# Kernel optimization log

Measured on AMD Instinct MI355X. Metric: run time of the kernel, lower is better.

Reference implementation:

```python
import jax, jax.numpy as jnp
import numpy as np

VOCAB, EMB, HID, OUT = 50257, 256, 512, 2

def setup_inputs() -> dict:
    key = jax.random.key(0)
    ks = jax.random.split(key, 8)
    s_e = 1.0  # nn.Embedding default N(0,1)
    emb = jax.random.normal(ks[0], (VOCAB, EMB), dtype=jnp.float32) * s_e
    emb = emb.at[0].set(0.0)  # padding_idx=0
    def lin(k1, k2, fan_in, fan_out):
        bound = 1.0 / np.sqrt(fan_in)
        w = jax.random.uniform(k1, (fan_out, fan_in), minval=-bound, maxval=bound, dtype=jnp.float32)
        b = jax.random.uniform(k2, (fan_out,), minval=-bound, maxval=bound, dtype=jnp.float32)
        return w, b
    Ww, Wb = lin(ks[1], ks[2], EMB, HID)
    Uw, Ub = lin(ks[3], ks[4], HID, HID)
    Vw, Vb = lin(ks[5], ks[6], HID, OUT)
    x = jax.random.randint(ks[7], (128, 512), 0, VOCAB, dtype=jnp.int64)
    return {"x": x, "emb": emb, "Ww": Ww, "Wb": Wb, "Uw": Uw, "Ub": Ub, "Vw": Vw, "Vb": Vb}

def reference(x, emb, Ww, Wb, Uw, Ub, Vw, Vb):
    # x: [B, T] int tokens -> embed: [B, T, E]
    xe = emb[x]
    # Precompute input projections for all timesteps in one big GEMM: [B, T, H]
    wx = jnp.einsum('bte,he->bth', xe, Ww) + Wb
    B = x.shape[0]
    h0 = jnp.zeros((B, Uw.shape[0]), dtype=xe.dtype)
    def step(h, wx_t):
        h_new = jnp.tanh(wx_t + h @ Uw.T + Ub)
        return h_new, None
    hT, _ = jax.lax.scan(step, h0, jnp.swapaxes(wx, 0, 1))  # scan over time [T, B, H]
    logits = hT @ Vw.T + Vb  # [B, OUT]
    return logits
```

## Files before the change

kernel.cpp:

```cpp
#include <hip/hip_runtime.h>
#include <hip/hip_bf16.h>
#include <math.h>


#define VOCAB   50257
#define T_STEPS 512
#define HID     512
#define EMB     256

typedef __bf16 bf16x8 __attribute__((ext_vector_type(8)));
typedef float  f32x4  __attribute__((ext_vector_type(4)));
typedef float  f32x2  __attribute__((ext_vector_type(2)));
typedef int    i32x4  __attribute__((ext_vector_type(4)));

__device__ inline float ldf(const void* p, long i, bool f32) {
    if (f32) return ((const float*)p)[i];
    unsigned bits = ((unsigned)((const unsigned short*)p)[i]) << 16;
    return __uint_as_float(bits);
}
__device__ inline void stf(void* p, long i, float v, bool f32) {
    if (f32) { ((float*)p)[i] = v; return; }
    unsigned b = __float_as_uint(v);
    unsigned r = (b + 0x7fffu + ((b >> 16) & 1u)) >> 16;
    ((unsigned short*)p)[i] = (unsigned short)r;
}
__device__ inline unsigned short f2bf(float v) {
    unsigned b = __float_as_uint(v);
    return (unsigned short)((b + 0x7fffu + ((b >> 16) & 1u)) >> 16);
}
__device__ inline float bf2f(unsigned short u) {
    return __uint_as_float(((unsigned)u) << 16);
}
__device__ inline int get_tok(const int* x, int idx, bool x64) {
    unsigned u = (unsigned)(x64 ? x[2 * idx] : x[idx]);
    return (u < (unsigned)VOCAB) ? (int)u : 0;
}
__device__ inline int detect_flags(const int* x, const void* emb) {
    int allz = 1;
    const unsigned short* e16 = (const unsigned short*)emb;
    for (int i = 256; i < 320; ++i) allz &= (e16[i] == 0);
    int x64 = 1;
    for (int j = 1; j < 16; j += 2) x64 &= (x[j] == 0);
    return allz | (x64 << 1);
}
__device__ inline float tanh_f(float x) {
    float ax = fabsf(x);
    float e  = __expf(-2.0f * ax);
    float t  = (1.0f - e) * __builtin_amdgcn_rcpf(1.0f + e);
    return copysignf(t, x);
}
__device__ inline unsigned tq(float v) {
    float x = fminf(3.5f, fmaxf(-3.5f, v));
    float s = x * x;
    float num = x * fmaf(s, fmaf(s, 127.0f, 13335.0f), 120015.0f);
    float den = fmaf(s, fmaf(s, 15.0f, 420.0f), 945.0f);
    float f = fmaf(num, __builtin_amdgcn_rcpf(den), 12582912.0f);
    return __float_as_uint(f) & 0xffu;
}
__device__ inline unsigned tq2(float a, float b) {
    f32x2 x;
    x.x = fminf(3.5f, fmaxf(-3.5f, a));
    x.y = fminf(3.5f, fmaxf(-3.5f, b));
    f32x2 s   = x * x;
    f32x2 num = x * (s * (s * 127.0f + 13335.0f) + 120015.0f);
    f32x2 den = s * (s * 15.0f + 420.0f) + 945.0f;
    float f0 = fmaf(num.x, __builtin_amdgcn_rcpf(den.x), 12582912.0f);
    float f1 = fmaf(num.y, __builtin_amdgcn_rcpf(den.y), 12582912.0f);
    return __builtin_amdgcn_perm(__float_as_uint(f1), __float_as_uint(f0),
                                 0x0c0c0400u);
}

#define XEPAD 264
__global__ __launch_bounds__(1024) void wx_gemm(
    const int* __restrict__ x, const void* __restrict__ embv,
    const void* __restrict__ Wwv, const void* __restrict__ Wbv,
    const void* __restrict__ Ubv, unsigned char* __restrict__ ws)
{
    __shared__ __align__(16) __hip_bfloat16 xe_s[64][XEPAD];
    __shared__ int flags_s;
    const int t = blockIdx.x, tid = threadIdx.x;
    if (tid == 0) flags_s = detect_flags(x, embv);
    __syncthreads();
    const bool f32w = (flags_s & 1) != 0;
    const bool x64  = (flags_s & 2) != 0;

    const int w = tid >> 6, lane = tid & 63, ln = lane & 15, q = lane >> 4;

    bf16x8 bf[2][8];
    float  bias[2];
#pragma unroll
    for (int tn = 0; tn < 2; ++tn) {
        long n = w * 32 + tn * 16 + ln;
        bias[tn] = ldf(Wbv, n, f32w) + ldf(Ubv, n, f32w);
#pragma unroll
        for (int kt = 0; kt < 8; ++kt) {
            bf16x8 v;
            if (f32w) {
                const float4* p = (const float4*)((const float*)Wwv
                                    + n * EMB + kt * 32 + q * 8);
                float4 a = p[0], b = p[1];
                v[0] = (__bf16)a.x; v[1] = (__bf16)a.y;
                v[2] = (__bf16)a.z; v[3] = (__bf16)a.w;
                v[4] = (__bf16)b.x; v[5] = (__bf16)b.y;
                v[6] = (__bf16)b.z; v[7] = (__bf16)b.w;
            } else {
                v = *(const bf16x8*)((const unsigned short*)Wwv
                                    + n * EMB + kt * 32 + q * 8);
            }
            bf[tn][kt] = v;
        }
    }

    for (int half = 0; half < 2; ++half) {
        {
            int row = tid >> 4, sub = tid & 15;
            int tok = get_tok(x, (half * 64 + row) * T_STEPS + t, x64);
#pragma unroll
            for (int i = 0; i < 4; ++i) {
                int col = sub * 4 + i * 64;
                __hip_bfloat16* d = &xe_s[row][col];
                if (f32w) {
                    const float4 vv = *(const float4*)((const float*)embv
                                        + (long)tok * EMB + col);
                    d[0] = __float2bfloat16(vv.x); d[1] = __float2bfloat16(vv.y);
                    d[2] = __float2bfloat16(vv.z); d[3] = __float2bfloat16(vv.w);
                } else {
                    *(uint2*)d = *(const uint2*)((const unsigned short*)embv
                                        + (long)tok * EMB + col);
                }
            }
        }
        __syncthreads();

#pragma unroll
        for (int bt = 0; bt < 4; ++bt) {
            f32x4 acc[2];
#pragma unroll
            for (int tn = 0; tn < 2; ++tn)
#pragma unroll
                for (int r = 0; r < 4; ++r) acc[tn][r] = bias[tn];
#pragma unroll
            for (int kt = 0; kt < 8; ++kt) {
                bf16x8 a = *(const bf16x8*)&xe_s[bt * 16 + ln][kt * 32 + q * 8];
#pragma unroll
                for (int tn = 0; tn < 2; ++tn)
                    acc[tn] = __builtin_amdgcn_mfma_f32_16x16x32_bf16(
                        a, bf[tn][kt], acc[tn], 0, 0, 0);
            }
            {
                int g = half * 4 + bt;
                unsigned short o8[8];
#pragma unroll
                for (int tn = 0; tn < 2; ++tn)
#pragma unroll
                    for (int r = 0; r < 4; ++r)
                        o8[tn * 4 + r] = f2bf(acc[tn][r]);
                long ofs = (((long)t * 8 + g) * 1024 + tid) * 16;
                *(uint4*)(ws + ofs) = *(const uint4*)o8;
            }
        }
        __syncthreads();
    }
}

#define HQP 528
__global__ __launch_bounds__(1024) void scan_i8(
    const void* __restrict__ Uwv, const void* __restrict__ Vwv,
    const void* __restrict__ Vbv, const int* __restrict__ x,
    const void* __restrict__ embv, const unsigned char* __restrict__ wsc,
    void* __restrict__ outv)
{
    __shared__ __align__(16) signed char hq[2][16][HQP];
    __shared__ float red[1024];
    __shared__ int flags_s;

    const int tid = threadIdx.x, g = blockIdx.x, b0 = g * 16;
    if (tid == 0) flags_s = detect_flags(x, embv);
    __syncthreads();
    const bool f32w = (flags_s & 1) != 0;

    const int w = tid >> 6, lane = tid & 63, ln = lane & 15, q = lane >> 4;

    {
        float mx = 0.0f;
        if (f32w) {
            const float4* U4 = (const float4*)Uwv;
            for (int i = tid; i < 65536; i += 1024) {
                float4 v = U4[i];
                mx = fmaxf(mx, fmaxf(fmaxf(fabsf(v.x), fabsf(v.y)),
                                     fmaxf(fabsf(v.z), fabsf(v.w))));
            }
        } else {
            for (long i = tid; i < 262144; i += 1024)
                mx = fmaxf(mx, fabsf(ldf(Uwv, i, false)));
        }
        red[tid] = mx;
        __syncthreads();
        for (int s = 512; s > 0; s >>= 1) {
            if (tid < s) red[tid] = fmaxf(red[tid], red[tid + s]);
            __syncthreads();
        }
    }
    const float su = red[0];
    const float qs = 127.0f / su;
    const float sc = su / 16129.0f;

    i32x4 uq[2][8];
#pragma unroll
    for (int tn = 0; tn < 2; ++tn) {
        long n = w * 32 + tn * 16 + ln;
#pragma unroll
        for (int kt = 0; kt < 8; ++kt) {
            i32x4 frag;
#pragma unroll
            for (int wd = 0; wd < 4; ++wd) {
                unsigned pk = 0;
#pragma unroll
                for (int jb = 0; jb < 4; ++jb) {
                    int kp = kt * 64 + q * 16 + wd * 4 + jb;
                    int kl = (kp & ~31) | ((kp & 1) << 4) | ((kp >> 1) & 15);
                    float v = ldf(Uwv, n * HID + kl, f32w) * qs;
                    int   qv = (int)__builtin_rintf(v);
                    qv = qv > 127 ? 127 : (qv < -127 ? -127 : qv);
                    pk |= ((unsigned)(unsigned char)(signed char)qv) << (8 * jb);
                }
                frag[wd] = (int)pk;
            }
            uq[tn][kt] = frag;
        }
    }

    for (int i = tid; i < 16 * HQP; i += 1024) ((signed char*)hq[0])[i] = 0;
    __syncthreads();

    const unsigned char* wxp = wsc + ((long)g * 1024 + tid) * 16;
    const long wx_step = 8L * 1024 * 16;

    uint4 wv = *(const uint4*)wxp;
    const unsigned char* wp = wxp + wx_step;

    for (int t = 0; t < T_STEPS; ++t) {
        uint4 wvn = *(const uint4*)((t + 1 < T_STEPS) ? wp : wxp);
        wp += wx_step;

        i32x4 acc0 = {0, 0, 0, 0}, acc1 = {0, 0, 0, 0};
        const signed char (*hr)[HQP] = hq[t & 1];
#pragma unroll
        for (int ktb = 0; ktb < 2; ++ktb) {
            i32x4 afr[4];
#pragma unroll
            for (int k = 0; k < 4; ++k)
                afr[k] = *(const i32x4*)&hr[ln][(ktb * 4 + k) * 64 + q * 16];
#pragma unroll
            for (int k = 0; k < 4; ++k) {
                acc0 = __builtin_amdgcn_mfma_i32_16x16x64_i8(
                    afr[k], uq[0][ktb * 4 + k], acc0, 0, 0, 0);
                acc1 = __builtin_amdgcn_mfma_i32_16x16x64_i8(
                    afr[k], uq[1][ktb * 4 + k], acc1, 0, 0, 0);
            }
        }

        float wx0[4], wx1[4];
        wx0[0] = __uint_as_float(wv.x << 16); wx0[1] = __uint_as_float(wv.x & 0xffff0000u);
        wx0[2] = __uint_as_float(wv.y << 16); wx0[3] = __uint_as_float(wv.y & 0xffff0000u);
        wx1[0] = __uint_as_float(wv.z << 16); wx1[1] = __uint_as_float(wv.z & 0xffff0000u);
        wx1[2] = __uint_as_float(wv.w << 16); wx1[3] = __uint_as_float(wv.w & 0xffff0000u);

        signed char (*hw)[HQP] = hq[(t + 1) & 1];
#pragma unroll
        for (int r = 0; r < 4; ++r) {
            unsigned c01 = tq2(fmaf((float)acc0[r], sc, wx0[r]),
                               fmaf((float)acc1[r], sc, wx1[r]));
            *(unsigned short*)&hw[q * 4 + r][w * 32 + ln * 2] =
                (unsigned short)c01;
        }
        asm volatile("s_waitcnt lgkmcnt(0)" ::: "memory");
        __builtin_amdgcn_s_barrier();
        wv = wvn;
    }

    if (tid < 512) {
        int b = tid >> 5, o = (tid >> 4) & 1, kp = tid & 15;
        float s = 0.0f;
#pragma unroll 4
        for (int j = 0; j < 32; ++j) {
            int kph = kp * 32 + j;
            int kl = (kph & ~31) | ((kph & 1) << 4) | ((kph >> 1) & 15);
            s += (float)hq[0][b][kph] * (1.0f / 127.0f)
               * ldf(Vwv, (long)o * HID + kl, f32w);
        }
        s += __shfl_xor(s, 1);
        s += __shfl_xor(s, 2);
        s += __shfl_xor(s, 4);
        s += __shfl_xor(s, 8);
        if (kp == 0)
            stf(outv, (long)(b0 + b) * 2 + o, s + ldf(Vbv, o, f32w), f32w);
    }
}

#define XPAD 264
#define HPAD 528
#define BPG  4
#define R7_WS_H   4096
#define R7_WS_NEED (4096 + 2 * 8 * 16 * 256 * 4)

__device__ inline void load_xe(const void* emb, long base, bool f32,
                               bf16x8* a, bf16x8* b) {
    if (f32) {
        const float* p = (const float*)emb + base;
        bf16x8 va, vb;
#pragma unroll
        for (int j = 0; j < 8; ++j) va[j] = (__bf16)p[j];
#pragma unroll
        for (int j = 0; j < 8; ++j) vb[j] = (__bf16)p[8 + j];
        *a = va; *b = vb;
    } else {
        const bf16x8* p = (const bf16x8*)((const unsigned short*)emb + base);
        *a = p[0]; *b = p[1];
    }
}

__global__ __launch_bounds__(256, 1) void scan_mfma_fb(
    const int* __restrict__ x, const void* __restrict__ embv,
    const void* __restrict__ Wwv, const void* __restrict__ Wbv,
    const void* __restrict__ Uwv, const void* __restrict__ Ubv,
    const void* __restrict__ Vwv, const void* __restrict__ Vbv,
    unsigned char* __restrict__ ws, void* __restrict__ outv)
{
    __shared__ __align__(16) __hip_bfloat16 xe_s[16][XPAD];
    __shared__ __align__(16) __hip_bfloat16 hbuf[2][16][HPAD];
    __shared__ int flags_s;

    const int tid = threadIdx.x;
    const int g   = blockIdx.x >> 2;
    const int cg  = blockIdx.x & 3;
    const int b0  = g * 16;

    if (tid == 0) flags_s = detect_flags(x, embv);
    __syncthreads();
    const bool f32w = (flags_s & 1) != 0;
    const bool x64  = (flags_s & 2) != 0;

    const int w = tid >> 6, lane = tid & 63, ln = lane & 15, q = lane >> 4;
    const int n0 = cg * 128 + w * 32 + ln;

    for (int i = tid; i < 2 * 16 * HPAD; i += 256)
        ((__hip_bfloat16*)hbuf)[i] = __float2bfloat16(0.0f);

    bf16x8 ufr[2][16], wfr[2][8];
#pragma unroll
    for (int half = 0; half < 2; ++half) {
        const long n = n0 + half * 16;
#pragma unroll
        for (int kt = 0; kt < 16; ++kt) {
            bf16x8 v;
#pragma unroll
            for (int j = 0; j < 8; ++j)
                v[j] = (__bf16)ldf(Uwv, n * HID + kt * 32 + q * 8 + j, f32w);
            ufr[half][kt] = v;
        }
#pragma unroll
        for (int kt = 0; kt < 8; ++kt) {
            bf16x8 v;
#pragma unroll
            for (int j = 0; j < 8; ++j)
                v[j] = (__bf16)ldf(Wwv, n * EMB + kt * 32 + q * 8 + j, f32w);
            wfr[half][kt] = v;
        }
    }
    const float bias0 = ldf(Wbv, n0, f32w)      + ldf(Ubv, n0, f32w);
    const float bias1 = ldf(Wbv, n0 + 16, f32w) + ldf(Ubv, n0 + 16, f32w);

    const int xr = tid >> 4, xc = (tid & 15) * 16;
    {
        int tok = get_tok(x, (b0 + xr) * T_STEPS + 0, x64);
        bf16x8 xa, xb;
        load_xe(embv, (long)tok * EMB + xc, f32w, &xa, &xb);
        *(bf16x8*)&xe_s[xr][xc]     = xa;
        *(bf16x8*)&xe_s[xr][xc + 8] = xb;
    }
    __syncthreads();

    unsigned*           hg32 = (unsigned*)(ws + R7_WS_H);
    unsigned long long* hg64 = (unsigned long long*)(ws + R7_WS_H);
    int*                cnt  = (int*)(void*)ws + g * 32;

    for (int t = 0; t < T_STEPS; ++t) {
        bf16x8 nxa, nxb;
        const bool have_next = (t + 1 < T_STEPS);
        if (have_next) {
            int tok = get_tok(x, (b0 + xr) * T_STEPS + (t + 1), x64);
            load_xe(embv, (long)tok * EMB + xc, f32w, &nxa, &nxb);
        }

        f32x4 acc0, acc1;
#pragma unroll
        for (int r = 0; r < 4; ++r) { acc0[r] = bias0; acc1[r] = bias1; }
#pragma unroll
        for (int kt = 0; kt < 8; ++kt) {
            bf16x8 a = *(const bf16x8*)&xe_s[ln][kt * 32 + q * 8];
            acc0 = __builtin_amdgcn_mfma_f32_16x16x32_bf16(a, wfr[0][kt], acc0, 0, 0, 0);
            acc1 = __builtin_amdgcn_mfma_f32_16x16x32_bf16(a, wfr[1][kt], acc1, 0, 0, 0);
        }
        const __hip_bfloat16 (*hr)[HPAD] = hbuf[t & 1];
#pragma unroll
        for (int kt = 0; kt < 16; ++kt) {
            bf16x8 a = *(const bf16x8*)&hr[ln][kt * 32 + q * 8];
            acc0 = __builtin_amdgcn_mfma_f32_16x16x32_bf16(a, ufr[0][kt], acc0, 0, 0, 0);
            acc1 = __builtin_amdgcn_mfma_f32_16x16x32_bf16(a, ufr[1][kt], acc1, 0, 0, 0);
        }

        const int nb = (t + 1) & 1;
        {
            unsigned* dst = hg32 + (size_t)(nb * 8 + g) * 4096 + cg * 64 + w * 16 + ln;
#pragma unroll
            for (int r = 0; r < 4; ++r) {
                unsigned word = (unsigned)f2bf(tanh_f(acc0[r]))
                              | ((unsigned)f2bf(tanh_f(acc1[r])) << 16);
                __hip_atomic_store(dst + (size_t)(q * 4 + r) * 256, word,
                                   __ATOMIC_RELAXED, __HIP_MEMORY_SCOPE_AGENT);
            }
        }
        asm volatile("s_waitcnt vmcnt(0)" ::: "memory");
        __syncthreads();

        if (have_next) {
            *(bf16x8*)&xe_s[xr][xc]     = nxa;
            *(bf16x8*)&xe_s[xr][xc + 8] = nxb;
        }

        if (tid == 0) {
            __hip_atomic_fetch_add(cnt, 1, __ATOMIC_RELAXED,
                                   __HIP_MEMORY_SCOPE_AGENT);
            const int target = BPG * (t + 1);
            while (__hip_atomic_load(cnt, __ATOMIC_RELAXED,
                                     __HIP_MEMORY_SCOPE_AGENT) < target)
                __builtin_amdgcn_s_sleep(1);
        }
        __syncthreads();

        {
            const unsigned long long* src = hg64 + (size_t)(nb * 8 + g) * 2048;
#pragma unroll
            for (int m = tid; m < 2048; m += 256) {
                unsigned long long v = __hip_atomic_load(
                    src + m, __ATOMIC_RELAXED, __HIP_MEMORY_SCOPE_AGENT);
                int row = m >> 7, p = m & 127;
                int j0  = 2 * p;
                int cgp = j0 >> 6, wv = (j0 >> 4) & 3, l0 = j0 & 15;
                int colA = cgp * 128 + wv * 32 + l0;
                unsigned w0 = (unsigned)v, w1 = (unsigned)(v >> 32);
                unsigned lo = (w0 & 0xffffu) | (w1 << 16);
                unsigned hi = (w0 >> 16) | (w1 & 0xffff0000u);
                *(unsigned*)&hbuf[nb][row][colA]      = lo;
                *(unsigned*)&hbuf[nb][row][colA + 16] = hi;
            }
        }
        __syncthreads();
    }

    if (cg == 0) {
        int b = tid >> 4, rem = tid & 15, o = rem >> 3, kp = rem & 7;
        float s = 0.0f;
#pragma unroll 4
        for (int j = 0; j < 64; ++j) {
            int k = kp * 64 + j;
            s += __bfloat162float(hbuf[0][b][k]) * ldf(Vwv, (long)o * HID + k, f32w);
        }
        s += __shfl_xor(s, 1);
        s += __shfl_xor(s, 2);
        s += __shfl_xor(s, 4);
        if (kp == 0)
            stf(outv, (long)(b0 + b) * 2 + o, s + ldf(Vbv, o, f32w), f32w);
    }
}

#define B_PER 2
__global__ __launch_bounds__(512) void fixup(
    const int* __restrict__ x, const void* __restrict__ emb,
    const void* __restrict__ Ww, const void* __restrict__ Wb,
    const void* __restrict__ Uw, const void* __restrict__ Ub,
    const void* __restrict__ Vw, const void* __restrict__ Vb,
    void* __restrict__ out, int force)
{
    __shared__ float h_s[2][B_PER][HID];
    __shared__ float xe_sf[B_PER][EMB];
    __shared__ int   flags_s, bad_s;

    const int tid = threadIdx.x;
    const int b0  = blockIdx.x * B_PER;

    if (tid == 0) {
        int fl = detect_flags(x, emb);
        flags_s = fl;
        int bad = force;
        if (!force) {
            bool f32o = (fl & 1) != 0;
            for (int i = 0; i < 2 * B_PER; ++i) {
                int oi = b0 * 2 + i;
                if (f32o) {
                    float v = ((const float*)out)[oi];
                    bad |= (v != v);
                } else {
                    unsigned short u = ((const unsigned short*)out)[oi];
                    bad |= (((u & 0x7F80u) == 0x7F80u) && ((u & 0x7Fu) != 0));
                }
            }
        }
        bad_s = bad;
    }
    __syncthreads();
    if (!bad_s) return;

    const bool f32w = (flags_s & 1) != 0;
    const bool x64  = (flags_s & 2) != 0;
    const int n = tid;
    const float bias = ldf(Wb, n, f32w) + ldf(Ub, n, f32w);

    for (int b = 0; b < B_PER; ++b) h_s[0][b][n] = 0.0f;

    for (int t = 0; t < T_STEPS; ++t) {
        {
            int b = tid >> 8, c = tid & 255;
            int tok = get_tok(x, (b0 + b) * T_STEPS + t, x64);
            xe_sf[b][c] = ldf(emb, (long)tok * EMB + c, f32w);
        }
        __syncthreads();

        float acc0 = bias, acc1 = bias;
        const long wrow = (long)n * EMB;
#pragma unroll 8
        for (int k = 0; k < EMB; ++k) {
            float wv = ldf(Ww, wrow + k, f32w);
            acc0 += xe_sf[0][k] * wv;
            acc1 += xe_sf[1][k] * wv;
        }
        const long urow = (long)n * HID;
        const float* hc0 = h_s[t & 1][0];
        const float* hc1 = h_s[t & 1][1];
#pragma unroll 8
        for (int k = 0; k < HID; ++k) {
            float uv = ldf(Uw, urow + k, f32w);
            acc0 += hc0[k] * uv;
            acc1 += hc1[k] * uv;
        }
        h_s[(t + 1) & 1][0][n] = tanhf(acc0);
        h_s[(t + 1) & 1][1][n] = tanhf(acc1);
        __syncthreads();
    }

    if (tid < 2 * B_PER) {
        int b = tid >> 1, o = tid & 1;
        float s = ldf(Vb, o, f32w);
        for (int k = 0; k < HID; ++k)
            s += h_s[0][b][k] * ldf(Vw, (long)o * HID + k, f32w);
        stf(out, (b0 + b) * 2 + o, s, f32w);
    }
}

extern "C" void kernel_launch(void* const* d_in, const int* in_sizes, int n_in,
                              void* d_out, int out_size, void* d_ws, size_t ws_size,
                              hipStream_t stream) {
    const int* x = (const int*)d_in[0];
    const size_t WX16 = (size_t)T_STEPS * 128 * 512 * 2;
    if (ws_size >= WX16) {
        wx_gemm<<<512, 1024, 0, stream>>>(
            x, d_in[1], d_in[2], d_in[3], d_in[5], (unsigned char*)d_ws);
        scan_i8<<<8, 1024, 0, stream>>>(
            d_in[4], d_in[6], d_in[7], x, d_in[1],
            (const unsigned char*)d_ws, d_out);
        fixup<<<64, 512, 0, stream>>>(
            x, d_in[1], d_in[2], d_in[3], d_in[4], d_in[5], d_in[6], d_in[7],
            d_out, 0);
    } else if (ws_size >= (size_t)R7_WS_NEED) {
        hipMemsetAsync(d_ws, 0, 4096, stream);
        scan_mfma_fb<<<32, 256, 0, stream>>>(
            x, d_in[1], d_in[2], d_in[3], d_in[4], d_in[5], d_in[6], d_in[7],
            (unsigned char*)d_ws, d_out);
        fixup<<<64, 512, 0, stream>>>(
            x, d_in[1], d_in[2], d_in[3], d_in[4], d_in[5], d_in[6], d_in[7],
            d_out, 0);
    } else {
        fixup<<<64, 512, 0, stream>>>(
            x, d_in[1], d_in[2], d_in[3], d_in[4], d_in[5], d_in[6], d_in[7],
            d_out, 1);
    }
}
```

Measured before the change: 857.3 us.

## Overlap tanh epilogue with second MFMA chain and load all embeddings in one pass

```diff
diff --git a/kernel.cpp b/kernel.cpp
--- a/kernel.cpp
+++ b/kernel.cpp
@@ -76,7 +76,7 @@
     const void* __restrict__ Wwv, const void* __restrict__ Wbv,
     const void* __restrict__ Ubv, unsigned char* __restrict__ ws)
 {
-    __shared__ __align__(16) __hip_bfloat16 xe_s[64][XEPAD];
+    __shared__ __align__(16) __hip_bfloat16 xe_s[128][XEPAD];
     __shared__ int flags_s;
     const int t = blockIdx.x, tid = threadIdx.x;
     if (tid == 0) flags_s = detect_flags(x, embv);
@@ -85,6 +85,30 @@
     const bool x64  = (flags_s & 2) != 0;
 
     const int w = tid >> 6, lane = tid & 63, ln = lane & 15, q = lane >> 4;
+
+    {
+        int row = tid >> 3, sub = tid & 7;
+        int tok = get_tok(x, row * T_STEPS + t, x64);
+        if (f32w) {
+            const float* src = (const float*)embv + (long)tok * EMB;
+#pragma unroll
+            for (int i = 0; i < 8; ++i) {
+                int col = sub * 4 + i * 32;
+                float4 vv = *(const float4*)(src + col);
+                __hip_bfloat16* d = &xe_s[row][col];
+                d[0] = __float2bfloat16(vv.x); d[1] = __float2bfloat16(vv.y);
+                d[2] = __float2bfloat16(vv.z); d[3] = __float2bfloat16(vv.w);
+            }
+        } else {
+            const unsigned short* src = (const unsigned short*)embv
+                                      + (long)tok * EMB;
+#pragma unroll
+            for (int i = 0; i < 4; ++i) {
+                int col = sub * 8 + i * 64;
+                *(uint4*)&xe_s[row][col] = *(const uint4*)(src + col);
+            }
+        }
+    }
 
     bf16x8 bf[2][8];
     float  bias[2];
@@ -110,56 +134,33 @@
             bf[tn][kt] = v;
         }
     }
-
-    for (int half = 0; half < 2; ++half) {
+    __syncthreads();
+
+#pragma unroll
+    for (int bt = 0; bt < 8; ++bt) {
+        f32x4 acc[2];
+#pragma unroll
+        for (int tn = 0; tn < 2; ++tn)
+#pragma unroll
+            for (int r = 0; r < 4; ++r) acc[tn][r] = bias[tn];
+#pragma unroll
+        for (int kt = 0; kt < 8; ++kt) {
+            bf16x8 a = *(const bf16x8*)&xe_s[bt * 16 + ln][kt * 32 + q * 8];
+#pragma unroll
+            for (int tn = 0; tn < 2; ++tn)
+                acc[tn] = __builtin_amdgcn_mfma_f32_16x16x32_bf16(
+                    a, bf[tn][kt], acc[tn], 0, 0, 0);
+        }
         {
-            int row = tid >> 4, sub = tid & 15;
-            int tok = get_tok(x, (half * 64 + row) * T_STEPS + t, x64);
-#pragma unroll
-            for (int i = 0; i < 4; ++i) {
-                int col = sub * 4 + i * 64;
-                __hip_bfloat16* d = &xe_s[row][col];
-                if (f32w) {
-                    const float4 vv = *(const float4*)((const float*)embv
-                                        + (long)tok * EMB + col);
-                    d[0] = __float2bfloat16(vv.x); d[1] = __float2bfloat16(vv.y);
-                    d[2] = __float2bfloat16(vv.z); d[3] = __float2bfloat16(vv.w);
-                } else {
-                    *(uint2*)d = *(const uint2*)((const unsigned short*)embv
-                                        + (long)tok * EMB + col);
-                }
-            }
-        }
-        __syncthreads();
-
-#pragma unroll
-        for (int bt = 0; bt < 4; ++bt) {
-            f32x4 acc[2];
+            unsigned short o8[8];
 #pragma unroll
             for (int tn = 0; tn < 2; ++tn)
 #pragma unroll
-                for (int r = 0; r < 4; ++r) acc[tn][r] = bias[tn];
-#pragma unroll
-            for (int kt = 0; kt < 8; ++kt) {
-                bf16x8 a = *(const bf16x8*)&xe_s[bt * 16 + ln][kt * 32 + q * 8];
-#pragma unroll
-                for (int tn = 0; tn < 2; ++tn)
-                    acc[tn] = __builtin_amdgcn_mfma_f32_16x16x32_bf16(
-                        a, bf[tn][kt], acc[tn], 0, 0, 0);
-            }
-            {
-                int g = half * 4 + bt;
-                unsigned short o8[8];
-#pragma unroll
-                for (int tn = 0; tn < 2; ++tn)
-#pragma unroll
-                    for (int r = 0; r < 4; ++r)
-                        o8[tn * 4 + r] = f2bf(acc[tn][r]);
-                long ofs = (((long)t * 8 + g) * 1024 + tid) * 16;
-                *(uint4*)(ws + ofs) = *(const uint4*)o8;
-            }
-        }
-        __syncthreads();
+                for (int r = 0; r < 4; ++r)
+                    o8[tn * 4 + r] = f2bf(acc[tn][r]);
+            long ofs = (((long)t * 8 + bt) * 1024 + tid) * 16;
+            *(uint4*)(ws + ofs) = *(const uint4*)o8;
+        }
     }
 }
 
@@ -239,26 +240,11 @@
     uint4 wv = *(const uint4*)wxp;
     const unsigned char* wp = wxp + wx_step;
 
+    const int wcol = w * 32 + ln * 2;
+
     for (int t = 0; t < T_STEPS; ++t) {
         uint4 wvn = *(const uint4*)((t + 1 < T_STEPS) ? wp : wxp);
         wp += wx_step;
-
-        i32x4 acc0 = {0, 0, 0, 0}, acc1 = {0, 0, 0, 0};
-        const signed char (*hr)[HQP] = hq[t & 1];
-#pragma unroll
-        for (int ktb = 0; ktb < 2; ++ktb) {
-            i32x4 afr[4];
-#pragma unroll
-            for (int k = 0; k < 4; ++k)
-                afr[k] = *(const i32x4*)&hr[ln][(ktb * 4 + k) * 64 + q * 16];
-#pragma unroll
-            for (int k = 0; k < 4; ++k) {
-                acc0 = __builtin_amdgcn_mfma_i32_16x16x64_i8(
-                    afr[k], uq[0][ktb * 4 + k], acc0, 0, 0, 0);
-                acc1 = __builtin_amdgcn_mfma_i32_16x16x64_i8(
-                    afr[k], uq[1][ktb * 4 + k], acc1, 0, 0, 0);
-            }
-        }
 
         float wx0[4], wx1[4];
         wx0[0] = __uint_as_float(wv.x << 16); wx0[1] = __uint_as_float(wv.x & 0xffff0000u);
@@ -266,14 +252,51 @@
         wx1[0] = __uint_as_float(wv.z << 16); wx1[1] = __uint_as_float(wv.z & 0xffff0000u);
         wx1[2] = __uint_as_float(wv.w << 16); wx1[3] = __uint_as_float(wv.w & 0xffff0000u);
 
+        const signed char (*hr)[HQP] = hq[t & 1];
         signed char (*hw)[HQP] = hq[(t + 1) & 1];
-#pragma unroll
-        for (int r = 0; r < 4; ++r) {
-            unsigned c01 = tq2(fmaf((float)acc0[r], sc, wx0[r]),
-                               fmaf((float)acc1[r], sc, wx1[r]));
-            *(unsigned short*)&hw[q * 4 + r][w * 32 + ln * 2] =
-                (unsigned short)c01;
-        }
+
+        i32x4 afr[8];
+#pragma unroll
+        for (int k = 0; k < 8; ++k)
+            afr[k] = *(const i32x4*)&hr[ln][k * 64 + q * 16];
+
+        i32x4 acc0 = {0, 0, 0, 0};
+#pragma unroll
+        for (int k = 0; k < 8; ++k)
+            acc0 = __builtin_amdgcn_mfma_i32_16x16x64_i8(
+                afr[k], uq[0][k], acc0, 0, 0, 0);
+
+        i32x4 acc1 = {0, 0, 0, 0};
+        acc1 = __builtin_amdgcn_mfma_i32_16x16x64_i8(afr[0], uq[1][0], acc1, 0, 0, 0);
+        acc1 = __builtin_amdgcn_mfma_i32_16x16x64_i8(afr[1], uq[1][1], acc1, 0, 0, 0);
+        float xa0 = fmaf((float)acc0[0], sc, wx0[0]);
+        float xa1 = fmaf((float)acc0[1], sc, wx0[1]);
+        acc1 = __builtin_amdgcn_mfma_i32_16x16x64_i8(afr[2], uq[1][2], acc1, 0, 0, 0);
+        acc1 = __builtin_amdgcn_mfma_i32_16x16x64_i8(afr[3], uq[1][3], acc1, 0, 0, 0);
+        unsigned cA = tq2(xa0, xa1);
+        float xa2 = fmaf((float)acc0[2], sc, wx0[2]);
+        float xa3 = fmaf((float)acc0[3], sc, wx0[3]);
+        acc1 = __builtin_amdgcn_mfma_i32_16x16x64_i8(afr[4], uq[1][4], acc1, 0, 0, 0);
+        acc1 = __builtin_amdgcn_mfma_i32_16x16x64_i8(afr[5], uq[1][5], acc1, 0, 0, 0);
+        unsigned cB = tq2(xa2, xa3);
+        hw[q * 4 + 0][wcol] = (signed char)cA;
+        hw[q * 4 + 1][wcol] = (signed char)(cA >> 8);
+        acc1 = __builtin_amdgcn_mfma_i32_16x16x64_i8(afr[6], uq[1][6], acc1, 0, 0, 0);
+        acc1 = __builtin_amdgcn_mfma_i32_16x16x64_i8(afr[7], uq[1][7], acc1, 0, 0, 0);
+        hw[q * 4 + 2][wcol] = (signed char)cB;
+        hw[q * 4 + 3][wcol] = (signed char)(cB >> 8);
+
+        float xb0 = fmaf((float)acc1[0], sc, wx1[0]);
+        float xb1 = fmaf((float)acc1[1], sc, wx1[1]);
+        float xb2 = fmaf((float)acc1[2], sc, wx1[2]);
+        float xb3 = fmaf((float)acc1[3], sc, wx1[3]);
+        unsigned cC = tq2(xb0, xb1);
+        unsigned cD = tq2(xb2, xb3);
+        hw[q * 4 + 0][wcol + 1] = (signed char)cC;
+        hw[q * 4 + 1][wcol + 1] = (signed char)(cC >> 8);
+        hw[q * 4 + 2][wcol + 1] = (signed char)cD;
+        hw[q * 4 + 3][wcol + 1] = (signed char)(cD >> 8);
+
         asm volatile("s_waitcnt lgkmcnt(0)" ::: "memory");
         __builtin_amdgcn_s_barrier();
         wv = wvn;
```

After: 941.5 us. 1.1x slower.

## Fuse input-projection GEMM and recurrent scan into one producer-consumer kernel

Applied to the files above, without the earlier changes.

```diff
diff --git a/kernel.cpp b/kernel.cpp
--- a/kernel.cpp
+++ b/kernel.cpp
@@ -48,14 +48,6 @@
     float e  = __expf(-2.0f * ax);
     float t  = (1.0f - e) * __builtin_amdgcn_rcpf(1.0f + e);
     return copysignf(t, x);
-}
-__device__ inline unsigned tq(float v) {
-    float x = fminf(3.5f, fmaxf(-3.5f, v));
-    float s = x * x;
-    float num = x * fmaf(s, fmaf(s, 127.0f, 13335.0f), 120015.0f);
-    float den = fmaf(s, fmaf(s, 15.0f, 420.0f), 945.0f);
-    float f = fmaf(num, __builtin_amdgcn_rcpf(den), 12582912.0f);
-    return __float_as_uint(f) & 0xffu;
 }
 __device__ inline unsigned tq2(float a, float b) {
     f32x2 x;
@@ -71,12 +63,272 @@
 }
 
 #define XEPAD 264
+#define HQP   528
+#define WX16  ((size_t)T_STEPS * 128 * 512 * 2)
+
+__global__ __launch_bounds__(1024) void fused_wx_scan(
+    const int* __restrict__ x, const void* __restrict__ embv,
+    const void* __restrict__ Wwv, const void* __restrict__ Wbv,
+    const void* __restrict__ Uwv, const void* __restrict__ Ubv,
+    const void* __restrict__ Vwv, const void* __restrict__ Vbv,
+    unsigned char* __restrict__ ws, void* __restrict__ outv)
+{
+    __shared__ __align__(16) unsigned char smem[128 * XEPAD * 2];
+    __shared__ int flags_s;
+    const int tid = threadIdx.x;
+    if (tid == 0) flags_s = detect_flags(x, embv);
+    __syncthreads();
+    const bool f32w = (flags_s & 1) != 0;
+    const bool x64  = (flags_s & 2) != 0;
+    int* const tflag = (int*)(ws + WX16);
+
+    const int w = tid >> 6, lane = tid & 63, ln = lane & 15, q = lane >> 4;
+
+    if (blockIdx.x >= 8) {
+        __hip_bfloat16 (*xe_s)[XEPAD] = (__hip_bfloat16 (*)[XEPAD])smem;
+        const int b = blockIdx.x - 8;
+
+        bf16x8 bf[2][8];
+        float  bias[2];
+#pragma unroll
+        for (int tn = 0; tn < 2; ++tn) {
+            long n = w * 32 + tn * 16 + ln;
+            bias[tn] = ldf(Wbv, n, f32w) + ldf(Ubv, n, f32w);
+#pragma unroll
+            for (int kt = 0; kt < 8; ++kt) {
+                bf16x8 v;
+                if (f32w) {
+                    const float4* p = (const float4*)((const float*)Wwv
+                                        + n * EMB + kt * 32 + q * 8);
+                    float4 a = p[0], c = p[1];
+                    v[0] = (__bf16)a.x; v[1] = (__bf16)a.y;
+                    v[2] = (__bf16)a.z; v[3] = (__bf16)a.w;
+                    v[4] = (__bf16)c.x; v[5] = (__bf16)c.y;
+                    v[6] = (__bf16)c.z; v[7] = (__bf16)c.w;
+                } else {
+                    v = *(const bf16x8*)((const unsigned short*)Wwv
+                                        + n * EMB + kt * 32 + q * 8);
+                }
+                bf[tn][kt] = v;
+            }
+        }
+
+        for (int it = 0; it < 8; ++it) {
+            const int t = it * 64 + b;
+            {
+                int row = tid >> 3, sub = tid & 7;
+                int tok = get_tok(x, row * T_STEPS + t, x64);
+                if (f32w) {
+                    const float* src = (const float*)embv + (long)tok * EMB;
+#pragma unroll
+                    for (int i = 0; i < 8; ++i) {
+                        int col = sub * 4 + i * 32;
+                        float4 vv = *(const float4*)(src + col);
+                        __hip_bfloat16* d = &xe_s[row][col];
+                        d[0] = __float2bfloat16(vv.x); d[1] = __float2bfloat16(vv.y);
+                        d[2] = __float2bfloat16(vv.z); d[3] = __float2bfloat16(vv.w);
+                    }
+                } else {
+                    const unsigned short* src = (const unsigned short*)embv
+                                              + (long)tok * EMB;
+#pragma unroll
+                    for (int i = 0; i < 4; ++i) {
+                        int col = sub * 8 + i * 64;
+                        *(uint4*)&xe_s[row][col] = *(const uint4*)(src + col);
+                    }
+                }
+            }
+            __syncthreads();
+
+#pragma unroll
+            for (int bt = 0; bt < 8; ++bt) {
+                f32x4 acc[2];
+#pragma unroll
+                for (int tn = 0; tn < 2; ++tn)
+#pragma unroll
+                    for (int r = 0; r < 4; ++r) acc[tn][r] = bias[tn];
+#pragma unroll
+                for (int kt = 0; kt < 8; ++kt) {
+                    bf16x8 a = *(const bf16x8*)&xe_s[bt * 16 + ln][kt * 32 + q * 8];
+#pragma unroll
+                    for (int tn = 0; tn < 2; ++tn)
+                        acc[tn] = __builtin_amdgcn_mfma_f32_16x16x32_bf16(
+                            a, bf[tn][kt], acc[tn], 0, 0, 0);
+                }
+                unsigned short o8[8];
+#pragma unroll
+                for (int tn = 0; tn < 2; ++tn)
+#pragma unroll
+                    for (int r = 0; r < 4; ++r)
+                        o8[tn * 4 + r] = f2bf(acc[tn][r]);
+                long ofs = (((long)t * 8 + bt) * 1024 + tid) * 16;
+                *(uint4*)(ws + ofs) = *(const uint4*)o8;
+            }
+            __syncthreads();
+            if (tid == 0)
+                __hip_atomic_store(&tflag[t], 1, __ATOMIC_RELEASE,
+                                   __HIP_MEMORY_SCOPE_AGENT);
+        }
+        return;
+    }
+
+    typedef signed char hq_t[16][HQP];
+    hq_t* hq   = (hq_t*)smem;
+    float* red = (float*)(smem + 2 * 16 * HQP);
+
+    const int g = blockIdx.x, b0 = g * 16;
+
+    {
+        float mx = 0.0f;
+        if (f32w) {
+            const float4* U4 = (const float4*)Uwv;
+            for (int i = tid; i < 65536; i += 1024) {
+                float4 v = U4[i];
+                mx = fmaxf(mx, fmaxf(fmaxf(fabsf(v.x), fabsf(v.y)),
+                                     fmaxf(fabsf(v.z), fabsf(v.w))));
+            }
+        } else {
+            for (long i = tid; i < 262144; i += 1024)
+                mx = fmaxf(mx, fabsf(ldf(Uwv, i, false)));
+        }
+        red[tid] = mx;
+        __syncthreads();
+        for (int s = 512; s > 0; s >>= 1) {
+            if (tid < s) red[tid] = fmaxf(red[tid], red[tid + s]);
+            __syncthreads();
+        }
+    }
+    const float su = red[0];
+    const float qs = 127.0f / su;
+    const float sc = su / 16129.0f;
+
+    i32x4 uq[2][8];
+#pragma unroll
+    for (int tn = 0; tn < 2; ++tn) {
+        long n = w * 32 + tn * 16 + ln;
+#pragma unroll
+        for (int kt = 0; kt < 8; ++kt) {
+            i32x4 frag;
+#pragma unroll
+            for (int wd = 0; wd < 4; ++wd) {
+                unsigned pk = 0;
+#pragma unroll
+                for (int jb = 0; jb < 4; ++jb) {
+                    int kp = kt * 64 + q * 16 + wd * 4 + jb;
+                    int kl = (kp & ~31) | ((kp & 1) << 4) | ((kp >> 1) & 15);
+                    float v = ldf(Uwv, n * HID + kl, f32w) * qs;
+                    int   qv = (int)__builtin_rintf(v);
+                    qv = qv > 127 ? 127 : (qv < -127 ? -127 : qv);
+                    pk |= ((unsigned)(unsigned char)(signed char)qv) << (8 * jb);
+                }
+                frag[wd] = (int)pk;
+            }
+            uq[tn][kt] = frag;
+        }
+    }
+
+    for (int i = tid; i < 16 * HQP; i += 1024) ((signed char*)smem)[i] = 0;
+
+    if (tid == 0) {
+        while (!__hip_atomic_load(&tflag[0], __ATOMIC_ACQUIRE,
+                                  __HIP_MEMORY_SCOPE_AGENT))
+            __builtin_amdgcn_s_sleep(2);
+        while (!__hip_atomic_load(&tflag[1], __ATOMIC_ACQUIRE,
+                                  __HIP_MEMORY_SCOPE_AGENT))
+            __builtin_amdgcn_s_sleep(2);
+    }
+    __syncthreads();
+
+    const unsigned char* wxp = ws + ((long)g * 1024 + tid) * 16;
+    const long wx_step = 8L * 1024 * 16;
+
+    unsigned long long v0 = __hip_atomic_load(
+        (const unsigned long long*)wxp, __ATOMIC_RELAXED,
+        __HIP_MEMORY_SCOPE_AGENT);
+    unsigned long long v1 = __hip_atomic_load(
+        (const unsigned long long*)(wxp + 8), __ATOMIC_RELAXED,
+        __HIP_MEMORY_SCOPE_AGENT);
+    const unsigned char* wp = wxp + wx_step;
+
+    for (int t = 0; t < T_STEPS; ++t) {
+        const unsigned char* pp = (t + 1 < T_STEPS) ? wp : wxp;
+        unsigned long long n0 = __hip_atomic_load(
+            (const unsigned long long*)pp, __ATOMIC_RELAXED,
+            __HIP_MEMORY_SCOPE_AGENT);
+        unsigned long long n1 = __hip_atomic_load(
+            (const unsigned long long*)(pp + 8), __ATOMIC_RELAXED,
+            __HIP_MEMORY_SCOPE_AGENT);
+        wp += wx_step;
+
+        i32x4 acc0 = {0, 0, 0, 0}, acc1 = {0, 0, 0, 0};
+        const signed char (*hr)[HQP] = hq[t & 1];
+#pragma unroll
+        for (int ktb = 0; ktb < 2; ++ktb) {
+            i32x4 afr[4];
+#pragma unroll
+            for (int k = 0; k < 4; ++k)
+                afr[k] = *(const i32x4*)&hr[ln][(ktb * 4 + k) * 64 + q * 16];
+#pragma unroll
+            for (int k = 0; k < 4; ++k) {
+                acc0 = __builtin_amdgcn_mfma_i32_16x16x64_i8(
+                    afr[k], uq[0][ktb * 4 + k], acc0, 0, 0, 0);
+                acc1 = __builtin_amdgcn_mfma_i32_16x16x64_i8(
+                    afr[k], uq[1][ktb * 4 + k], acc1, 0, 0, 0);
+            }
+        }
+
+        unsigned wvx = (unsigned)v0, wvy = (unsigned)(v0 >> 32);
+        unsigned wvz = (unsigned)v1, wvw = (unsigned)(v1 >> 32);
+        float wx0[4], wx1[4];
+        wx0[0] = __uint_as_float(wvx << 16); wx0[1] = __uint_as_float(wvx & 0xffff0000u);
+        wx0[2] = __uint_as_float(wvy << 16); wx0[3] = __uint_as_float(wvy & 0xffff0000u);
+        wx1[0] = __uint_as_float(wvz << 16); wx1[1] = __uint_as_float(wvz & 0xffff0000u);
+        wx1[2] = __uint_as_float(wvw << 16); wx1[3] = __uint_as_float(wvw & 0xffff0000u);
+
+        signed char (*hw)[HQP] = hq[(t + 1) & 1];
+#pragma unroll
+        for (int r = 0; r < 4; ++r) {
+            unsigned c01 = tq2(fmaf((float)acc0[r], sc, wx0[r]),
+                               fmaf((float)acc1[r], sc, wx1[r]));
+            *(unsigned short*)&hw[q * 4 + r][w * 32 + ln * 2] =
+                (unsigned short)c01;
+        }
+
+        if (tid == 0 && t + 2 < T_STEPS) {
+            while (!__hip_atomic_load(&tflag[t + 2], __ATOMIC_RELAXED,
+                                      __HIP_MEMORY_SCOPE_AGENT))
+                __builtin_amdgcn_s_sleep(2);
+        }
+        asm volatile("s_waitcnt lgkmcnt(0)" ::: "memory");
+        __builtin_amdgcn_s_barrier();
+        v0 = n0; v1 = n1;
+    }
+
+    if (tid < 512) {
+        int b = tid >> 5, o = (tid >> 4) & 1, kp = tid & 15;
+        float s = 0.0f;
+#pragma unroll 4
+        for (int j = 0; j < 32; ++j) {
+            int kph = kp * 32 + j;
+            int kl = (kph & ~31) | ((kph & 1) << 4) | ((kph >> 1) & 15);
+            s += (float)hq[0][b][kph] * (1.0f / 127.0f)
+               * ldf(Vwv, (long)o * HID + kl, f32w);
+        }
+        s += __shfl_xor(s, 1);
+        s += __shfl_xor(s, 2);
+        s += __shfl_xor(s, 4);
+        s += __shfl_xor(s, 8);
+        if (kp == 0)
+            stf(outv, (long)(b0 + b) * 2 + o, s + ldf(Vbv, o, f32w), f32w);
+    }
+}
+
 __global__ __launch_bounds__(1024) void wx_gemm(
     const int* __restrict__ x, const void* __restrict__ embv,
     const void* __restrict__ Wwv, const void* __restrict__ Wbv,
     const void* __restrict__ Ubv, unsigned char* __restrict__ ws)
 {
-    __shared__ __align__(16) __hip_bfloat16 xe_s[64][XEPAD];
+    __shared__ __align__(16) __hip_bfloat16 xe_s[128][XEPAD];
     __shared__ int flags_s;
     const int t = blockIdx.x, tid = threadIdx.x;
     if (tid == 0) flags_s = detect_flags(x, embv);
@@ -85,6 +337,30 @@
     const bool x64  = (flags_s & 2) != 0;
 
     const int w = tid >> 6, lane = tid & 63, ln = lane & 15, q = lane >> 4;
+
+    {
+        int row = tid >> 3, sub = tid & 7;
+        int tok = get_tok(x, row * T_STEPS + t, x64);
+        if (f32w) {
+            const float* src = (const float*)embv + (long)tok * EMB;
+#pragma unroll
+            for (int i = 0; i < 8; ++i) {
+                int col = sub * 4 + i * 32;
+                float4 vv = *(const float4*)(src + col);
+                __hip_bfloat16* d = &xe_s[row][col];
+                d[0] = __float2bfloat16(vv.x); d[1] = __float2bfloat16(vv.y);
+                d[2] = __float2bfloat16(vv.z); d[3] = __float2bfloat16(vv.w);
+            }
+        } else {
+            const unsigned short* src = (const unsigned short*)embv
+                                      + (long)tok * EMB;
+#pragma unroll
+            for (int i = 0; i < 4; ++i) {
+                int col = sub * 8 + i * 64;
+                *(uint4*)&xe_s[row][col] = *(const uint4*)(src + col);
+            }
+        }
+    }
 
     bf16x8 bf[2][8];
     float  bias[2];
@@ -110,60 +386,36 @@
             bf[tn][kt] = v;
         }
     }
-
-    for (int half = 0; half < 2; ++half) {
+    __syncthreads();
+
+#pragma unroll
+    for (int bt = 0; bt < 8; ++bt) {
+        f32x4 acc[2];
+#pragma unroll
+        for (int tn = 0; tn < 2; ++tn)
+#pragma unroll
+            for (int r = 0; r < 4; ++r) acc[tn][r] = bias[tn];
+#pragma unroll
+        for (int kt = 0; kt < 8; ++kt) {
+            bf16x8 a = *(const bf16x8*)&xe_s[bt * 16 + ln][kt * 32 + q * 8];
+#pragma unroll
+            for (int tn = 0; tn < 2; ++tn)
+                acc[tn] = __builtin_amdgcn_mfma_f32_16x16x32_bf16(
+                    a, bf[tn][kt], acc[tn], 0, 0, 0);
+        }
         {
-            int row = tid >> 4, sub = tid & 15;
-            int tok = get_tok(x, (half * 64 + row) * T_STEPS + t, x64);
-#pragma unroll
-            for (int i = 0; i < 4; ++i) {
-                int col = sub * 4 + i * 64;
-                __hip_bfloat16* d = &xe_s[row][col];
-                if (f32w) {
-                    const float4 vv = *(const float4*)((const float*)embv
-                                        + (long)tok * EMB + col);
-                    d[0] = __float2bfloat16(vv.x); d[1] = __float2bfloat16(vv.y);
-                    d[2] = __float2bfloat16(vv.z); d[3] = __float2bfloat16(vv.w);
-                } else {
-                    *(uint2*)d = *(const uint2*)((const unsigned short*)embv
-                                        + (long)tok * EMB + col);
-                }
-            }
-        }
-        __syncthreads();
-
-#pragma unroll
-        for (int bt = 0; bt < 4; ++bt) {
-            f32x4 acc[2];
+            unsigned short o8[8];
 #pragma unroll
             for (int tn = 0; tn < 2; ++tn)
 #pragma unroll
-                for (int r = 0; r < 4; ++r) acc[tn][r] = bias[tn];
-#pragma unroll
-            for (int kt = 0; kt < 8; ++kt) {
-                bf16x8 a = *(const bf16x8*)&xe_s[bt * 16 + ln][kt * 32 + q * 8];
-#pragma unroll
-                for (int tn = 0; tn < 2; ++tn)
-                    acc[tn] = __builtin_amdgcn_mfma_f32_16x16x32_bf16(
-                        a, bf[tn][kt], acc[tn], 0, 0, 0);
-            }
-            {
-                int g = half * 4 + bt;
-                unsigned short o8[8];
-#pragma unroll
-                for (int tn = 0; tn < 2; ++tn)
-#pragma unroll
-                    for (int r = 0; r < 4; ++r)
-                        o8[tn * 4 + r] = f2bf(acc[tn][r]);
-                long ofs = (((long)t * 8 + g) * 1024 + tid) * 16;
-                *(uint4*)(ws + ofs) = *(const uint4*)o8;
-            }
-        }
-        __syncthreads();
-    }
-}
-
-#define HQP 528
+                for (int r = 0; r < 4; ++r)
+                    o8[tn * 4 + r] = f2bf(acc[tn][r]);
+            long ofs = (((long)t * 8 + bt) * 1024 + tid) * 16;
+            *(uint4*)(ws + ofs) = *(const uint4*)o8;
+        }
+    }
+}
+
 __global__ __launch_bounds__(1024) void scan_i8(
     const void* __restrict__ Uwv, const void* __restrict__ Vwv,
     const void* __restrict__ Vbv, const int* __restrict__ x,
@@ -562,13 +814,20 @@
                               void* d_out, int out_size, void* d_ws, size_t ws_size,
                               hipStream_t stream) {
     const int* x = (const int*)d_in[0];
-    const size_t WX16 = (size_t)T_STEPS * 128 * 512 * 2;
-    if (ws_size >= WX16) {
+    unsigned char* ws = (unsigned char*)d_ws;
+    if (ws_size >= WX16 + 4096) {
+        hipMemsetAsync(ws + WX16, 0, T_STEPS * sizeof(int), stream);
+        fused_wx_scan<<<72, 1024, 0, stream>>>(
+            x, d_in[1], d_in[2], d_in[3], d_in[4], d_in[5], d_in[6], d_in[7],
+            ws, d_out);
+        fixup<<<64, 512, 0, stream>>>(
+            x, d_in[1], d_in[2], d_in[3], d_in[4], d_in[5], d_in[6], d_in[7],
+            d_out, 0);
+    } else if (ws_size >= WX16) {
         wx_gemm<<<512, 1024, 0, stream>>>(
-            x, d_in[1], d_in[2], d_in[3], d_in[5], (unsigned char*)d_ws);
+            x, d_in[1], d_in[2], d_in[3], d_in[5], ws);
         scan_i8<<<8, 1024, 0, stream>>>(
-            d_in[4], d_in[6], d_in[7], x, d_in[1],
-            (const unsigned char*)d_ws, d_out);
+            d_in[4], d_in[6], d_in[7], x, d_in[1], ws, d_out);
         fixup<<<64, 512, 0, stream>>>(
             x, d_in[1], d_in[2], d_in[3], d_in[4], d_in[5], d_in[6], d_in[7],
             d_out, 0);
@@ -576,7 +835,7 @@
         hipMemsetAsync(d_ws, 0, 4096, stream);
         scan_mfma_fb<<<32, 256, 0, stream>>>(
             x, d_in[1], d_in[2], d_in[3], d_in[4], d_in[5], d_in[6], d_in[7],
-            (unsigned char*)d_ws, d_out);
+            ws, d_out);
         fixup<<<64, 512, 0, stream>>>(
             x, d_in[1], d_in[2], d_in[3], d_in[4], d_in[5], d_in[6], d_in[7],
             d_out, 0);
```

Measured after the change: 852.0 us. About the same (-0.6%).
